# Kernel optimization log

Hardware: AMD Instinct MI355X
Metric: run time of the kernel (lower is better)

## Reference

```python
import jax, jax.numpy as jnp
import numpy as np

# Dimensions per init_kwargs
B, S, D = 2, 2048, 1024          # batch, seq, hidden_size
F = 4096                          # intermediate_size
E, K = 8, 2                       # moe_num_experts, moe_top_k
EPS = 1e-9


def setup_inputs() -> dict:
    key = jax.random.key(0)
    k1, k2, k3, k4 = jax.random.split(key, 4)
    x = jax.random.normal(k1, (B, S, D), dtype=jnp.float32)
    # gate: Linear(D, E, bias=False) -> stored as [D, E] for x @ w_gate
    w_gate = jax.random.normal(k2, (D, E), dtype=jnp.float32) * 0.02
    # per-expert gate_up_proj: Linear(D, 2F, bias=False), stacked over experts -> [E, D, 2F]
    w_gate_up = jax.random.normal(k3, (E, D, 2 * F), dtype=jnp.float32) * 0.02
    # per-expert down_proj: Linear(F, D, bias=False), stacked -> [E, F, D]
    w_down = jax.random.normal(k4, (E, F, D), dtype=jnp.float32) * 0.02
    return {"x": x, "w_gate": w_gate, "w_gate_up": w_gate_up, "w_down": w_down}


def reference(x, w_gate, w_gate_up, w_down):
    # Router
    gate_logits = x @ w_gate                       # [B,S,E]
    gate_probs = jax.nn.softmax(gate_logits, axis=-1)
    # top-k masking + renormalization (top_k < num_experts)
    topk_vals, topk_idx = jax.lax.top_k(gate_probs, K)           # [B,S,K]
    masked = jnp.sum(jax.nn.one_hot(topk_idx, E, dtype=gate_probs.dtype)
                     * topk_vals[..., None], axis=-2)            # [B,S,E]
    denom = jnp.maximum(jnp.sum(masked, axis=-1, keepdims=True), EPS)
    gate_probs = masked / denom

    # Dense per-expert SwiGLU FFN on all tokens (faithful to reference impl)
    gu = jnp.einsum('bsd,edh->ebsh', x, w_gate_up)               # [E,B,S,2F]
    g, u = jnp.split(gu, 2, axis=-1)                             # [E,B,S,F] each
    act = jax.nn.silu(g) * u                                     # [E,B,S,F]
    expert_out = jnp.einsum('ebsf,efd->ebsd', act, w_down)       # [E,B,S,D]

    # Gate-weighted combine
    return jnp.einsum('bse,ebsd->bsd', gate_probs, expert_out)   # [B,S,D]
```

## Files before the change

### kernel.cpp

```cpp
#include <hip/hip_runtime.h>
#include <stdint.h>

#define NTOK 4096
#define DMODEL 1024
#define FF 4096
#define NEXP 8

typedef __bf16 bf16x8 __attribute__((ext_vector_type(8)));
typedef float f32x4 __attribute__((ext_vector_type(4)));

__device__ __forceinline__ unsigned short f2bf(float f) {
  union { float f; unsigned u; } v; v.f = f;
  unsigned r = v.u + 0x7fffu + ((v.u >> 16) & 1u);
  return (unsigned short)(r >> 16);
}

__global__ __launch_bounds__(256) void k_convert_x(const float4* __restrict__ in,
                                                   ushort4* __restrict__ out, int n4) {
  int stride = gridDim.x * blockDim.x;
  for (int i = blockIdx.x * blockDim.x + threadIdx.x; i < n4; i += stride) {
    float4 v = in[i];
    out[i] = make_ushort4(f2bf(v.x), f2bf(v.y), f2bf(v.z), f2bf(v.w));
  }
}

__global__ __launch_bounds__(256) void k_transpose_bf16(const float* __restrict__ in,
                                                        unsigned short* __restrict__ out,
                                                        int R, int C) {
  __shared__ float tile[64][65];
  const size_t slab = (size_t)R * C;
  const float* ip = in + slab * blockIdx.z;
  unsigned short* op = out + slab * blockIdx.z;
  int c0 = blockIdx.x * 64, r0 = blockIdx.y * 64;
  int tx = threadIdx.x & 15, ty = threadIdx.x >> 4;
#pragma unroll
  for (int i = 0; i < 4; ++i) {
    int r = ty + 16 * i;
    float4 v = *(const float4*)(ip + (size_t)(r0 + r) * C + c0 + tx * 4);
    tile[r][tx * 4 + 0] = v.x;
    tile[r][tx * 4 + 1] = v.y;
    tile[r][tx * 4 + 2] = v.z;
    tile[r][tx * 4 + 3] = v.w;
  }
  __syncthreads();
#pragma unroll
  for (int i = 0; i < 4; ++i) {
    int q = ty + 16 * i;
    ushort4 o = make_ushort4(f2bf(tile[tx * 4 + 0][q]), f2bf(tile[tx * 4 + 1][q]),
                             f2bf(tile[tx * 4 + 2][q]), f2bf(tile[tx * 4 + 3][q]));
    *(ushort4*)(op + (size_t)(c0 + q) * R + r0 + tx * 4) = o;
  }
}

__global__ __launch_bounds__(256) void k_router(const float* __restrict__ x,
                                                const float* __restrict__ wg,
                                                int* __restrict__ cnt,
                                                int* __restrict__ elist,
                                                float* __restrict__ gw) {
  int wave = threadIdx.x >> 6, lane = threadIdx.x & 63;
  int t = blockIdx.x * 4 + wave;
  const float* xp = x + (size_t)t * DMODEL;
  float a[8] = {0, 0, 0, 0, 0, 0, 0, 0};
#pragma unroll
  for (int i = 0; i < DMODEL / 64; ++i) {
    int d = lane + 64 * i;
    float xv = xp[d];
    float4 w0 = *(const float4*)(wg + d * 8);
    float4 w1 = *(const float4*)(wg + d * 8 + 4);
    a[0] += xv * w0.x; a[1] += xv * w0.y; a[2] += xv * w0.z; a[3] += xv * w0.w;
    a[4] += xv * w1.x; a[5] += xv * w1.y; a[6] += xv * w1.z; a[7] += xv * w1.w;
  }
#pragma unroll
  for (int off = 32; off > 0; off >>= 1)
#pragma unroll
    for (int e = 0; e < 8; ++e) a[e] += __shfl_down(a[e], off, 64);
  if (lane == 0) {
    int e0 = 0;
    for (int e = 1; e < 8; ++e) if (a[e] > a[e0]) e0 = e;
    int e1 = (e0 == 0) ? 1 : 0;
    for (int e = 0; e < 8; ++e) if (e != e0 && a[e] > a[e1]) e1 = e;
    float p = __expf(a[e1] - a[e0]);
    float inv = 1.0f / (1.0f + p);
    int p0 = atomicAdd(&cnt[e0], 1);
    elist[e0 * NTOK + p0] = 2 * t;
    gw[2 * t] = inv;
    int p1 = atomicAdd(&cnt[e1], 1);
    elist[e1 * NTOK + p1] = 2 * t + 1;
    gw[2 * t + 1] = p * inv;
  }
}

__global__ __launch_bounds__(512, 2) void k_gemm1(const unsigned short* __restrict__ xb,
                                                  const unsigned short* __restrict__ wgu,
                                                  const int* __restrict__ cnt,
                                                  const int* __restrict__ elist,
                                                  unsigned short* __restrict__ act)
{
  __shared__ __align__(16) unsigned short sA[2][256 * 64];
  __shared__ __align__(16) unsigned short sB[2][256 * 64];

  const int e = blockIdx.z;
  const int n_e = cnt[e];
  const int m0 = blockIdx.y * 256;
  if (m0 >= n_e) return;
  const int c0 = blockIdx.x * 128;
  const int tid = threadIdx.x;
  const int w = tid >> 6, lane = tid & 63;
  const int wr = w >> 2, wc = w & 3;
  const int* el = elist + e * NTOK;
  const int csub = ((lane & 7) ^ (lane >> 3)) * 8;
  const int srow = w * 8 + (lane >> 3);

  int tokrow[4];
  size_t baddr[4];
  const unsigned short* wb = wgu + (size_t)e * (2 * FF) * DMODEL;
#pragma unroll
  for (int i = 0; i < 4; ++i) {
    int r = i * 64 + srow;
    int idx = m0 + r;
    tokrow[i] = el[idx < n_e ? idx : 0] >> 1;
    int strip = r >> 6, off = r & 63;
    int wrow = (off < 32) ? (c0 + strip * 32 + off) : (FF + c0 + strip * 32 + off - 32);
    baddr[i] = (size_t)wrow * DMODEL;
  }

  f32x4 acc[8][4];
  f32x4 zero = {0.f, 0.f, 0.f, 0.f};
#pragma unroll
  for (int m = 0; m < 8; ++m)
#pragma unroll
    for (int n = 0; n < 4; ++n) acc[m][n] = zero;

  auto stage = [&](int buf, int k0) {
#pragma unroll
    for (int i = 0; i < 4; ++i) {
      const unsigned short* g = xb + (size_t)tokrow[i] * DMODEL + k0 + csub;
      __builtin_amdgcn_global_load_lds((const __attribute__((address_space(1))) void*)g,
                                       (__attribute__((address_space(3))) void*)(&sA[buf][(i * 64 + w * 8) * 64]),
                                       16, 0, 0);
    }
#pragma unroll
    for (int i = 0; i < 4; ++i) {
      const unsigned short* g = wb + baddr[i] + k0 + csub;
      __builtin_amdgcn_global_load_lds((const __attribute__((address_space(1))) void*)g,
                                       (__attribute__((address_space(3))) void*)(&sB[buf][(i * 64 + w * 8) * 64]),
                                       16, 0, 0);
    }
  };

  auto compute = [&](int buf) {
#pragma unroll
    for (int kk = 0; kk < 2; ++kk) {
      const int xk = ((kk * 4 + (lane >> 4)) ^ (lane & 7)) * 8;
      bf16x8 af[8], bf[4];
#pragma unroll
      for (int m = 0; m < 8; ++m)
        af[m] = *(const bf16x8*)(&sA[buf][(wr * 128 + m * 16 + (lane & 15)) * 64 + xk]);
#pragma unroll
      for (int n = 0; n < 4; ++n)
        bf[n] = *(const bf16x8*)(&sB[buf][(wc * 64 + n * 16 + (lane & 15)) * 64 + xk]);
#pragma unroll
      for (int m = 0; m < 8; ++m)
#pragma unroll
        for (int n = 0; n < 4; ++n)
          acc[m][n] = __builtin_amdgcn_mfma_f32_16x16x32_bf16(af[m], bf[n], acc[m][n], 0, 0, 0);
    }
  };

  stage(0, 0);
  __syncthreads();
  int cur = 0;
  for (int t = 0; t < DMODEL / 64; ++t) {
    if (t + 1 < DMODEL / 64) stage(cur ^ 1, (t + 1) * 64);
    compute(cur);
    __syncthreads();
    cur ^= 1;
  }

#pragma unroll
  for (int m = 0; m < 8; ++m) {
#pragma unroll
    for (int r = 0; r < 4; ++r) {
      int idx = m0 + wr * 128 + m * 16 + (lane >> 4) * 4 + r;
      if (idx < n_e) {
        int p = el[idx];
        unsigned short* ap = act + (size_t)p * FF + c0 + wc * 32;
#pragma unroll
        for (int n = 0; n < 2; ++n) {
          float g = acc[m][n][r];
          float u = acc[m][n + 2][r];
          float s = g / (1.0f + __expf(-g));
          ap[n * 16 + (lane & 15)] = f2bf(s * u);
        }
      }
    }
  }
}

__global__ __launch_bounds__(256) void k_gemm2(const unsigned short* __restrict__ actb,
                                               const unsigned short* __restrict__ wd,
                                               const int* __restrict__ cnt,
                                               const int* __restrict__ elist,
                                               const float* __restrict__ gw,
                                               float* __restrict__ out_slot)
{
  __shared__ __align__(16) unsigned short sA[128 * 64];
  __shared__ __align__(16) unsigned short sB[128 * 64];

  const int e = blockIdx.z;
  const int n_e = cnt[e];
  const int m0 = blockIdx.y * 128;
  if (m0 >= n_e) return;
  const int n0 = blockIdx.x * 128;
  const int tid = threadIdx.x;
  const int w = tid >> 6, lane = tid & 63;
  const int wr = w >> 1, wc = w & 1;
  const int* el = elist + e * NTOK;
  const int csub = ((lane & 7) ^ (lane >> 3)) * 8;

  int prow[4];
  size_t baddr[4];
  const unsigned short* wb = wd + (size_t)e * DMODEL * FF;
#pragma unroll
  for (int i = 0; i < 4; ++i) {
    int r = i * 32 + w * 8 + (lane >> 3);
    int idx = m0 + r;
    prow[i] = el[idx < n_e ? idx : 0];
    baddr[i] = (size_t)(n0 + r) * FF;
  }

  f32x4 acc[4][4];
  f32x4 zero = {0.f, 0.f, 0.f, 0.f};
#pragma unroll
  for (int m = 0; m < 4; ++m)
#pragma unroll
    for (int n = 0; n < 4; ++n) acc[m][n] = zero;

  for (int k0 = 0; k0 < FF; k0 += 64) {
#pragma unroll
    for (int i = 0; i < 4; ++i) {
      const unsigned short* g = actb + (size_t)prow[i] * FF + k0 + csub;
      __builtin_amdgcn_global_load_lds((const __attribute__((address_space(1))) void*)g,
                                       (__attribute__((address_space(3))) void*)(&sA[(i * 32 + w * 8) * 64]),
                                       16, 0, 0);
    }
#pragma unroll
    for (int i = 0; i < 4; ++i) {
      const unsigned short* g = wb + baddr[i] + k0 + csub;
      __builtin_amdgcn_global_load_lds((const __attribute__((address_space(1))) void*)g,
                                       (__attribute__((address_space(3))) void*)(&sB[(i * 32 + w * 8) * 64]),
                                       16, 0, 0);
    }
    __syncthreads();
#pragma unroll
    for (int kk = 0; kk < 2; ++kk) {
      const int xk = ((kk * 4 + (lane >> 4)) ^ (lane & 7)) * 8;
      bf16x8 af[4], bf[4];
#pragma unroll
      for (int m = 0; m < 4; ++m)
        af[m] = *(const bf16x8*)(&sA[(wr * 64 + m * 16 + (lane & 15)) * 64 + xk]);
#pragma unroll
      for (int n = 0; n < 4; ++n)
        bf[n] = *(const bf16x8*)(&sB[(wc * 64 + n * 16 + (lane & 15)) * 64 + xk]);
#pragma unroll
      for (int m = 0; m < 4; ++m)
#pragma unroll
        for (int n = 0; n < 4; ++n)
          acc[m][n] = __builtin_amdgcn_mfma_f32_16x16x32_bf16(af[m], bf[n], acc[m][n], 0, 0, 0);
    }
    __syncthreads();
  }

#pragma unroll
  for (int m = 0; m < 4; ++m) {
#pragma unroll
    for (int r = 0; r < 4; ++r) {
      int idx = m0 + wr * 64 + m * 16 + (lane >> 4) * 4 + r;
      if (idx < n_e) {
        int p = el[idx];
        float wgt = gw[p];
        float* op = out_slot + (size_t)p * DMODEL + n0 + wc * 64;
#pragma unroll
        for (int n = 0; n < 4; ++n)
          op[n * 16 + (lane & 15)] = acc[m][n][r] * wgt;
      }
    }
  }
}

__global__ __launch_bounds__(256) void k_combine(const float4* __restrict__ slot,
                                                 float4* __restrict__ out, int n4) {
  int stride = gridDim.x * blockDim.x;
  for (int i = blockIdx.x * blockDim.x + threadIdx.x; i < n4; i += stride) {
    int t = i >> 8;
    int j = i & 255;
    float4 a = slot[(size_t)(2 * t) * 256 + j];
    float4 b = slot[(size_t)(2 * t + 1) * 256 + j];
    float4 o;
    o.x = a.x + b.x; o.y = a.y + b.y; o.z = a.z + b.z; o.w = a.w + b.w;
    out[i] = o;
  }
}

extern "C" void kernel_launch(void* const* d_in, const int* in_sizes, int n_in,
                              void* d_out, int out_size, void* d_ws, size_t ws_size,
                              hipStream_t stream) {
  const float* x   = (const float*)d_in[0];
  const float* wg  = (const float*)d_in[1];
  const float* wgu = (const float*)d_in[2];
  const float* wd  = (const float*)d_in[3];
  float* out = (float*)d_out;

  char* ws = (char*)d_ws;
  size_t off = 0;
  auto alloc = [&](size_t bytes) -> char* {
    char* p = ws + off;
    off += (bytes + 255) & ~(size_t)255;
    return p;
  };
  unsigned short* wgu_t = (unsigned short*)alloc((size_t)NEXP * 2 * FF * DMODEL * 2);
  unsigned short* wd_t  = (unsigned short*)alloc((size_t)NEXP * DMODEL * FF * 2);
  unsigned short* actb  = (unsigned short*)alloc((size_t)2 * NTOK * FF * 2);
  float* out_slot       = (float*)alloc((size_t)2 * NTOK * DMODEL * 4);
  unsigned short* xb    = (unsigned short*)alloc((size_t)NTOK * DMODEL * 2);
  int* elist            = (int*)alloc((size_t)NEXP * NTOK * 4);
  float* gw             = (float*)alloc((size_t)2 * NTOK * 4);
  int* cnt              = (int*)alloc(256);
  if (off > ws_size) return;

  hipMemsetAsync(cnt, 0, 256, stream);
  k_convert_x<<<1024, 256, 0, stream>>>((const float4*)x, (ushort4*)xb, NTOK * DMODEL / 4);
  k_transpose_bf16<<<dim3(2 * FF / 64, DMODEL / 64, NEXP), 256, 0, stream>>>(wgu, wgu_t, DMODEL, 2 * FF);
  k_transpose_bf16<<<dim3(DMODEL / 64, FF / 64, NEXP), 256, 0, stream>>>(wd, wd_t, FF, DMODEL);
  k_router<<<NTOK / 4, 256, 0, stream>>>(x, wg, cnt, elist, gw);
  k_gemm1<<<dim3(FF / 128, NTOK / 256, NEXP), 512, 0, stream>>>(xb, wgu_t, cnt, elist, actb);
  k_gemm2<<<dim3(DMODEL / 128, NTOK / 128, NEXP), 256, 0, stream>>>(actb, wd_t, cnt, elist, gw, out_slot);
  k_combine<<<2048, 256, 0, stream>>>((const float4*)out_slot, (float4*)out, NTOK * DMODEL / 4);
}
```

Measured before the change: 619.3 us.

## Interleave gemm1 prefetch with MFMA phases and remap gate/up weight layout

Splits the gemm1 k-loop into four sub-phases that each load fragments, issue part of the next tile's global-to-LDS prefetch, and run MFMAs under raised priority, with explicit vmcnt waits and barriers. The gate/up weight transpose now writes gate and up rows in contiguous 256-row blocks per 128-column tile, which simplifies B addressing. The goal is finer overlap of memory loads with matrix math. The cost is more barriers per k-step and reliance on hand-counted vmcnt values.

```diff
diff --git a/kernel.cpp b/kernel.cpp
--- a/kernel.cpp
+++ b/kernel.cpp
@@ -26,7 +26,7 @@
 
 __global__ __launch_bounds__(256) void k_transpose_bf16(const float* __restrict__ in,
                                                         unsigned short* __restrict__ out,
-                                                        int R, int C) {
+                                                        int R, int C, int remap) {
   __shared__ float tile[64][65];
   const size_t slab = (size_t)R * C;
   const float* ip = in + slab * blockIdx.z;
@@ -46,9 +46,18 @@
 #pragma unroll
   for (int i = 0; i < 4; ++i) {
     int q = ty + 16 * i;
+    int oc = c0 + q;
+    int orow;
+    if (remap) {
+      int up = (oc >= FF);
+      int cc = oc - up * FF;
+      orow = (cc >> 7) * 256 + up * 128 + (cc & 127);
+    } else {
+      orow = oc;
+    }
     ushort4 o = make_ushort4(f2bf(tile[tx * 4 + 0][q]), f2bf(tile[tx * 4 + 1][q]),
                              f2bf(tile[tx * 4 + 2][q]), f2bf(tile[tx * 4 + 3][q]));
-    *(ushort4*)(op + (size_t)(c0 + q) * R + r0 + tx * 4) = o;
+    *(ushort4*)(op + (size_t)orow * R + r0 + tx * 4) = o;
   }
 }
 
@@ -103,25 +112,23 @@
   const int n_e = cnt[e];
   const int m0 = blockIdx.y * 256;
   if (m0 >= n_e) return;
-  const int c0 = blockIdx.x * 128;
+  const int x = blockIdx.x;
+  const int c0 = x * 128;
   const int tid = threadIdx.x;
   const int w = tid >> 6, lane = tid & 63;
   const int wr = w >> 2, wc = w & 3;
   const int* el = elist + e * NTOK;
   const int csub = ((lane & 7) ^ (lane >> 3)) * 8;
-  const int srow = w * 8 + (lane >> 3);
 
   int tokrow[4];
   size_t baddr[4];
   const unsigned short* wb = wgu + (size_t)e * (2 * FF) * DMODEL;
 #pragma unroll
   for (int i = 0; i < 4; ++i) {
-    int r = i * 64 + srow;
+    int r = i * 64 + w * 8 + (lane >> 3);
     int idx = m0 + r;
     tokrow[i] = el[idx < n_e ? idx : 0] >> 1;
-    int strip = r >> 6, off = r & 63;
-    int wrow = (off < 32) ? (c0 + strip * 32 + off) : (FF + c0 + strip * 32 + off - 32);
-    baddr[i] = (size_t)wrow * DMODEL;
+    baddr[i] = (size_t)(x * 256 + r) * DMODEL;
   }
 
   f32x4 acc[8][4];
@@ -131,16 +138,18 @@
 #pragma unroll
     for (int n = 0; n < 4; ++n) acc[m][n] = zero;
 
-  auto stage = [&](int buf, int k0) {
-#pragma unroll
-    for (int i = 0; i < 4; ++i) {
+  auto stageA = [&](int buf, int k0, int h) {
+#pragma unroll
+    for (int i = 2 * h; i < 2 * h + 2; ++i) {
       const unsigned short* g = xb + (size_t)tokrow[i] * DMODEL + k0 + csub;
       __builtin_amdgcn_global_load_lds((const __attribute__((address_space(1))) void*)g,
                                        (__attribute__((address_space(3))) void*)(&sA[buf][(i * 64 + w * 8) * 64]),
                                        16, 0, 0);
     }
-#pragma unroll
-    for (int i = 0; i < 4; ++i) {
+  };
+  auto stageB = [&](int buf, int k0, int h) {
+#pragma unroll
+    for (int i = 2 * h; i < 2 * h + 2; ++i) {
       const unsigned short* g = wb + baddr[i] + k0 + csub;
       __builtin_amdgcn_global_load_lds((const __attribute__((address_space(1))) void*)g,
                                        (__attribute__((address_space(3))) void*)(&sB[buf][(i * 64 + w * 8) * 64]),
@@ -148,49 +157,72 @@
     }
   };
 
-  auto compute = [&](int buf) {
-#pragma unroll
-    for (int kk = 0; kk < 2; ++kk) {
-      const int xk = ((kk * 4 + (lane >> 4)) ^ (lane & 7)) * 8;
-      bf16x8 af[8], bf[4];
-#pragma unroll
-      for (int m = 0; m < 8; ++m)
-        af[m] = *(const bf16x8*)(&sA[buf][(wr * 128 + m * 16 + (lane & 15)) * 64 + xk]);
-#pragma unroll
-      for (int n = 0; n < 4; ++n)
-        bf[n] = *(const bf16x8*)(&sB[buf][(wc * 64 + n * 16 + (lane & 15)) * 64 + xk]);
-#pragma unroll
-      for (int m = 0; m < 8; ++m)
-#pragma unroll
-        for (int n = 0; n < 4; ++n)
-          acc[m][n] = __builtin_amdgcn_mfma_f32_16x16x32_bf16(af[m], bf[n], acc[m][n], 0, 0, 0);
-    }
-  };
-
-  stage(0, 0);
-  __syncthreads();
-  int cur = 0;
-  for (int t = 0; t < DMODEL / 64; ++t) {
-    if (t + 1 < DMODEL / 64) stage(cur ^ 1, (t + 1) * 64);
-    compute(cur);
-    __syncthreads();
-    cur ^= 1;
-  }
-
-#pragma unroll
-  for (int m = 0; m < 8; ++m) {
-#pragma unroll
-    for (int r = 0; r < 4; ++r) {
-      int idx = m0 + wr * 128 + m * 16 + (lane >> 4) * 4 + r;
-      if (idx < n_e) {
-        int p = el[idx];
-        unsigned short* ap = act + (size_t)p * FF + c0 + wc * 32;
-#pragma unroll
-        for (int n = 0; n < 2; ++n) {
-          float g = acc[m][n][r];
-          float u = acc[m][n + 2][r];
-          float s = g / (1.0f + __expf(-g));
-          ap[n * 16 + (lane & 15)] = f2bf(s * u);
+  const int NT = DMODEL / 64;
+  stageA(0, 0, 0); stageB(0, 0, 0); stageA(0, 0, 1); stageB(0, 0, 1);
+  asm volatile("s_waitcnt vmcnt(4)" ::: "memory");
+  __builtin_amdgcn_s_barrier();
+
+  for (int t = 0; t < NT; ++t) {
+    const int buf = t & 1;
+    const int nk0 = (t + 1) * 64;
+    const bool pre = (t + 1 < NT);
+#pragma unroll
+    for (int p = 0; p < 4; ++p) {
+      const int mh = p & 1, nh = p >> 1;
+      bf16x8 af[4][2], bfr[2][2];
+#pragma unroll
+      for (int kk = 0; kk < 2; ++kk) {
+        const int xk = ((kk * 4 + (lane >> 4)) ^ (lane & 7)) * 8;
+#pragma unroll
+        for (int m = 0; m < 4; ++m)
+          af[m][kk] = *(const bf16x8*)(&sA[buf][(mh * 128 + wr * 64 + m * 16 + (lane & 15)) * 64 + xk]);
+#pragma unroll
+        for (int n = 0; n < 2; ++n)
+          bfr[n][kk] = *(const bf16x8*)(&sB[buf][(nh * 128 + wc * 32 + n * 16 + (lane & 15)) * 64 + xk]);
+      }
+      if (pre) {
+        if (p & 1) stageB(buf ^ 1, nk0, p >> 1);
+        else       stageA(buf ^ 1, nk0, p >> 1);
+      }
+      __builtin_amdgcn_s_barrier();
+      __builtin_amdgcn_s_setprio(1);
+#pragma unroll
+      for (int kk = 0; kk < 2; ++kk)
+#pragma unroll
+        for (int m = 0; m < 4; ++m)
+#pragma unroll
+          for (int n = 0; n < 2; ++n)
+            acc[mh * 4 + m][nh * 2 + n] =
+                __builtin_amdgcn_mfma_f32_16x16x32_bf16(af[m][kk], bfr[n][kk],
+                                                        acc[mh * 4 + m][nh * 2 + n], 0, 0, 0);
+      __builtin_amdgcn_s_setprio(0);
+      if (pre) {
+        if (p != 2) asm volatile("s_waitcnt vmcnt(4)" ::: "memory");
+      } else {
+        if (p == 0) asm volatile("s_waitcnt vmcnt(2)" ::: "memory");
+        else if (p == 1) asm volatile("s_waitcnt vmcnt(0)" ::: "memory");
+      }
+      __builtin_amdgcn_s_barrier();
+    }
+  }
+
+#pragma unroll
+  for (int mh = 0; mh < 2; ++mh) {
+#pragma unroll
+    for (int m = 0; m < 4; ++m) {
+#pragma unroll
+      for (int r = 0; r < 4; ++r) {
+        int idx = m0 + mh * 128 + wr * 64 + m * 16 + (lane >> 4) * 4 + r;
+        if (idx < n_e) {
+          int p = el[idx];
+          unsigned short* ap = act + (size_t)p * FF + c0 + wc * 32;
+#pragma unroll
+          for (int n = 0; n < 2; ++n) {
+            float g = acc[mh * 4 + m][n][r];
+            float u = acc[mh * 4 + m][n + 2][r];
+            float s = g / (1.0f + __expf(-g));
+            ap[n * 16 + (lane & 15)] = f2bf(s * u);
+          }
         }
       }
     }
@@ -330,8 +362,8 @@
 
   hipMemsetAsync(cnt, 0, 256, stream);
   k_convert_x<<<1024, 256, 0, stream>>>((const float4*)x, (ushort4*)xb, NTOK * DMODEL / 4);
-  k_transpose_bf16<<<dim3(2 * FF / 64, DMODEL / 64, NEXP), 256, 0, stream>>>(wgu, wgu_t, DMODEL, 2 * FF);
-  k_transpose_bf16<<<dim3(DMODEL / 64, FF / 64, NEXP), 256, 0, stream>>>(wd, wd_t, FF, DMODEL);
+  k_transpose_bf16<<<dim3(2 * FF / 64, DMODEL / 64, NEXP), 256, 0, stream>>>(wgu, wgu_t, DMODEL, 2 * FF, 1);
+  k_transpose_bf16<<<dim3(DMODEL / 64, FF / 64, NEXP), 256, 0, stream>>>(wd, wd_t, FF, DMODEL, 0);
   k_router<<<NTOK / 4, 256, 0, stream>>>(x, wg, cnt, elist, gw);
   k_gemm1<<<dim3(FF / 128, NTOK / 256, NEXP), 512, 0, stream>>>(xb, wgu_t, cnt, elist, actb);
   k_gemm2<<<dim3(DMODEL / 128, NTOK / 128, NEXP), 256, 0, stream>>>(actb, wd_t, cnt, elist, gw, out_slot);
```

Result: slower. 648.7 us (+4.7%).
